# Kernel optimization log

Measured on AMD Instinct MI355X. Metric: run time of the kernel, lower is better.

The kernel has to match this reference:

```python
import jax, jax.numpy as jnp
import numpy as np

N = 100000   # nodes
C = 16       # num_classes
G = 2        # number of graphs (meta-paths)
L = 2        # PLP layers
E = 3200000  # edges per graph
F = 512      # feature dim
H = 64       # mlp hidden dim


def setup_inputs() -> dict:
    key = jax.random.key(0)
    ks = jax.random.split(key, 13)
    return {
        "features": jax.random.normal(ks[0], (N, F), jnp.float32),
        "label_init": jax.random.uniform(ks[1], (N, C), jnp.float32),
        "labels_one_hot": jax.random.uniform(ks[2], (N, C), jnp.float32),
        "alpha": jax.random.normal(ks[3], (N, 1), jnp.float32),
        "attention": jax.random.normal(ks[4], (N, G, 1), jnp.float32),
        "e_edge": jax.random.normal(ks[5], (L, G, E), jnp.float32),
        "w1": jax.random.normal(ks[6], (F, H), jnp.float32) * 0.05,
        "b1": jnp.zeros((H,), jnp.float32),
        "w2": jax.random.normal(ks[7], (H, C), jnp.float32) * 0.05,
        "b2": jnp.zeros((C,), jnp.float32),
        "src": jax.random.randint(ks[8], (G, E), 0, N, jnp.int32),
        "dst": jax.random.randint(ks[9], (G, E), 0, N, jnp.int32),
        "train_mask": jax.random.randint(ks[10], (N, 1), 0, 2, jnp.int32),
    }


def edge_softmax(e, dst, n):
    # softmax of per-edge logits over edges sharing the same destination node
    m = jax.ops.segment_max(e, dst, num_segments=n)          # [N]
    ex = jnp.exp(e - m[dst])                                  # [E]
    s = jax.ops.segment_sum(ex, dst, num_segments=n)          # [N]
    return ex / s[dst]


def reference(features, label_init, labels_one_hot, alpha, attention,
              e_edge, w1, b1, w2, b2, src, dst, train_mask):
    mask = train_mask.astype(jnp.float32)            # [N,1] 1 = train node
    masked_label = 1.0 - mask                         # (~masked).float()
    masked_one_hot = labels_one_hot * mask            # clamp train labels

    h_list = []
    for i in range(G):
        h = label_init
        for l in range(L):
            a = edge_softmax(e_edge[l, i], dst[i], N)         # [E]
            msg = h[src[i]] * a[:, None]                       # u_mul_e: [E,C]
            h = jax.ops.segment_sum(msg, dst[i], num_segments=N)  # fn.sum
            h = h * masked_label + masked_one_hot
        h_list.append(h)

    x = jnp.stack(h_list, axis=-1)                    # [N,C,G]
    att = jax.nn.softmax(attention, axis=1)[..., 0]   # [N,G]
    logits = jnp.einsum('ncg,ng->nc', x, att)         # [N,C]

    mlp_out = jax.nn.relu(features @ w1 + b1) @ w2 + b2   # MLP2, 2 layers
    return jax.nn.sigmoid(alpha) * logits + jax.nn.sigmoid(-alpha) * mlp_out
```

## Files before the change

### kernel.cpp

```cpp
#include <hip/hip_runtime.h>

#define NN 100000
#define CC 16
#define GG 2
#define LL 2
#define EE 3200000
#define FF 512
#define HH 64
#define GN (GG * NN)
#define GE (GG * EE)
#define CAPE (GE / 5 * 3)

#define SCAN_TILE 1024
#define SCAN_NB ((GN + SCAN_TILE - 1) / SCAN_TILE)

struct Pay { int src; float ex0; float ex1; };


__global__ __launch_bounds__(256) void count_kernel(
    const int* __restrict__ dst, const int* __restrict__ mask,
    int* __restrict__ deg)
{
    int t = blockIdx.x * 256 + threadIdx.x;
    int d = dst[t];
    if (mask[d] == 0) {
        int m = (t < EE ? 0 : NN) + d;
        atomicAdd(&deg[m], 1);
    }
}

__global__ __launch_bounds__(256) void scan_partial_kernel(
    const int* __restrict__ deg, int* __restrict__ bsum)
{
    __shared__ int lds[256];
    int t = threadIdx.x;
    int base = blockIdx.x * SCAN_TILE + t * 4;
    int s = 0;
    if (base + 3 < GN) {
        int4 v = *(const int4*)(deg + base);
        s = v.x + v.y + v.z + v.w;
    } else {
        for (int i = 0; i < 4; i++) if (base + i < GN) s += deg[base + i];
    }
    lds[t] = s;
    __syncthreads();
    for (int off = 128; off > 0; off >>= 1) {
        if (t < off) lds[t] += lds[t + off];
        __syncthreads();
    }
    if (t == 0) bsum[blockIdx.x] = lds[0];
}

__global__ __launch_bounds__(256) void scan_bsum_kernel(
    int* __restrict__ bsum, int* __restrict__ ptr)
{
    __shared__ int lds[256];
    int t = threadIdx.x;
    int v = (t < SCAN_NB) ? bsum[t] : 0;
    lds[t] = v;
    __syncthreads();
    for (int off = 1; off < 256; off <<= 1) {
        int y = (t >= off) ? lds[t - off] : 0;
        __syncthreads();
        lds[t] += y;
        __syncthreads();
    }
    if (t == 255) ptr[GN] = lds[255];
    bsum[t] = lds[t] - v;
}

__global__ __launch_bounds__(256) void scan_final_kernel(
    int* __restrict__ deg, const int* __restrict__ bsum, int* __restrict__ ptr)
{
    __shared__ int lds[256];
    int t = threadIdx.x;
    int base = blockIdx.x * SCAN_TILE + t * 4;
    int d0 = 0, d1 = 0, d2 = 0, d3 = 0;
    if (base + 3 < GN) {
        int4 v = *(const int4*)(deg + base);
        d0 = v.x; d1 = v.y; d2 = v.z; d3 = v.w;
    } else {
        if (base + 0 < GN) d0 = deg[base + 0];
        if (base + 1 < GN) d1 = deg[base + 1];
        if (base + 2 < GN) d2 = deg[base + 2];
        if (base + 3 < GN) d3 = deg[base + 3];
    }
    int s = d0 + d1 + d2 + d3;
    lds[t] = s;
    __syncthreads();
    for (int off = 1; off < 256; off <<= 1) {
        int y = (t >= off) ? lds[t - off] : 0;
        __syncthreads();
        lds[t] += y;
        __syncthreads();
    }
    int run = bsum[blockIdx.x] + lds[t] - s;
    if (base + 0 < GN) { ptr[base + 0] = run; deg[base + 0] = run; } run += d0;
    if (base + 1 < GN) { ptr[base + 1] = run; deg[base + 1] = run; } run += d1;
    if (base + 2 < GN) { ptr[base + 2] = run; deg[base + 2] = run; } run += d2;
    if (base + 3 < GN) { ptr[base + 3] = run; deg[base + 3] = run; }
}

__global__ __launch_bounds__(256) void scatter_kernel(
    const int* __restrict__ dst, const int* __restrict__ src,
    const float* __restrict__ e0, const float* __restrict__ e1,
    const int* __restrict__ mask, int* __restrict__ cursor,
    Pay* __restrict__ pay)
{
    int t = blockIdx.x * 256 + threadIdx.x;
    int d = dst[t];
    if (mask[d] != 0) return;
    int m = (t < EE ? 0 : NN) + d;
    int p = atomicAdd(&cursor[m], 1);
    if (p < CAPE) {
        Pay pv;
        pv.src = src[t];
        pv.ex0 = __expf(e0[t]);
        pv.ex1 = __expf(e1[t]);
        pay[p] = pv;
    }
}

__global__ __launch_bounds__(256) void gather_kernel(
    const Pay* __restrict__ pay, const int* __restrict__ ptr,
    const float* __restrict__ hs0, const float* __restrict__ hs1,
    const int* __restrict__ mask, const float* __restrict__ one_hot,
    float* __restrict__ hout, int layer)
{
    int m    = (blockIdx.x * 256 + threadIdx.x) >> 6;
    int lane = threadIdx.x & 63;
    int c    = lane & 15;
    int sub  = lane >> 4;
    int g    = (m < NN) ? 0 : 1;
    int n    = m - g * NN;

    if (mask[n]) {
        if (sub == 0) hout[m * CC + c] = one_hot[n * CC + c];
        return;
    }

    const float* hs = g ? hs1 : hs0;
    int beg = ptr[m], end = ptr[m + 1];
    float acc = 0.f, s = 0.f;
    for (int j = beg + sub; j < end; j += 4) {
        Pay pv = pay[j];
        float ex = layer ? pv.ex1 : pv.ex0;
        s   += ex;
        acc += ex * hs[pv.src * CC + c];
    }
    acc += __shfl_xor(acc, 16);
    acc += __shfl_xor(acc, 32);
    s   += __shfl_xor(s, 16);
    s   += __shfl_xor(s, 32);
    if (sub == 0)
        hout[m * CC + c] = (s > 0.f) ? acc / s : 0.f;
}

__global__ __launch_bounds__(256) void edge_kernel(
    const float* __restrict__ e, const int* __restrict__ src,
    const int* __restrict__ dst, const float* __restrict__ hs0,
    const float* __restrict__ hs1, float* __restrict__ hn,
    float* __restrict__ s)
{
    int t = blockIdx.x * 256 + threadIdx.x;
    int edge = t >> 4;
    int c = t & 15;
    float ev = e[edge];
    int sv = src[edge];
    int dv = dst[edge];
    float ex = __expf(ev);
    const float* hs;
    int hbase, sbase;
    if (edge < EE) { hs = hs0; hbase = 0;       sbase = 0;  }
    else           { hs = hs1; hbase = NN * CC; sbase = NN; }
    float val = hs[sv * CC + c] * ex;
    atomicAdd(&hn[hbase + dv * CC + c], val);
    if (c == 0) atomicAdd(&s[sbase + dv], ex);
}

__global__ __launch_bounds__(256) void update_kernel(
    const float* __restrict__ hn, const float* __restrict__ s,
    const int* __restrict__ train_mask, const float* __restrict__ labels_one_hot,
    float* __restrict__ hc)
{
    int idx = blockIdx.x * 256 + threadIdx.x;
    int n = idx >> 4;
    float mask = (float)train_mask[n];
    float ml = 1.0f - mask;
    float lab = labels_one_hot[idx] * mask;
#pragma unroll
    for (int g = 0; g < GG; g++) {
        float sv = s[g * NN + n];
        float x = (sv > 0.0f) ? hn[g * NN * CC + idx] / sv : 0.0f;
        hc[g * NN * CC + idx] = x * ml + lab;
    }
}

#define MLP_ROWS 128
__global__ __launch_bounds__(256) void mlp_combine_kernel(
    const float* __restrict__ feat, const float* __restrict__ w1,
    const float* __restrict__ b1, const float* __restrict__ w2,
    const float* __restrict__ b2, const float* __restrict__ hc,
    const float* __restrict__ attention, const float* __restrict__ alpha,
    float* __restrict__ out)
{
    __shared__ float smem[9792];
    float* sA  = smem;
    float* sB  = smem + 4224;
    float* sh1 = smem;
    float* sw2 = smem + 8704;

    int t = threadIdx.x;
    int row0 = blockIdx.x * MLP_ROWS;
    int rg = t >> 4;
    int cg = t & 15;

    for (int i = t; i < HH * CC; i += 256)
        sw2[(i >> 4) * 17 + (i & 15)] = w2[i];

    float acc[8][4];
#pragma unroll
    for (int r = 0; r < 8; r++)
#pragma unroll
        for (int c = 0; c < 4; c++) acc[r][c] = 0.0f;

    for (int kt = 0; kt < FF; kt += 32) {
#pragma unroll
        for (int i = 0; i < 4; i++) {
            int s4 = t + i * 256;
            int r  = s4 >> 3;
            int k4 = (s4 & 7) << 2;
            int grow = row0 + r;
            float4 v = make_float4(0.f, 0.f, 0.f, 0.f);
            if (grow < NN)
                v = *(const float4*)(feat + (size_t)grow * FF + kt + k4);
            sA[(k4 + 0) * 132 + r] = v.x;
            sA[(k4 + 1) * 132 + r] = v.y;
            sA[(k4 + 2) * 132 + r] = v.z;
            sA[(k4 + 3) * 132 + r] = v.w;
        }
#pragma unroll
        for (int i = 0; i < 2; i++) {
            int s4 = t + i * 256;
            int k  = s4 >> 4;
            int c4 = (s4 & 15) << 2;
            float4 wv = *(const float4*)(w1 + (size_t)(kt + k) * HH + c4);
            *(float4*)&sB[k * 68 + c4] = wv;
        }
        __syncthreads();
#pragma unroll 8
        for (int k = 0; k < 32; k++) {
            float4 a0 = *(const float4*)&sA[k * 132 + rg * 8];
            float4 a1 = *(const float4*)&sA[k * 132 + rg * 8 + 4];
            float4 b  = *(const float4*)&sB[k * 68 + cg * 4];
            float ar[8] = {a0.x, a0.y, a0.z, a0.w, a1.x, a1.y, a1.z, a1.w};
            float bc[4] = {b.x, b.y, b.z, b.w};
#pragma unroll
            for (int r = 0; r < 8; r++)
#pragma unroll
                for (int c = 0; c < 4; c++) acc[r][c] += ar[r] * bc[c];
        }
        __syncthreads();
    }

    float4 bb = *(const float4*)(b1 + cg * 4);
#pragma unroll
    for (int r = 0; r < 8; r++) {
        float4 hv;
        hv.x = fmaxf(acc[r][0] + bb.x, 0.f);
        hv.y = fmaxf(acc[r][1] + bb.y, 0.f);
        hv.z = fmaxf(acc[r][2] + bb.z, 0.f);
        hv.w = fmaxf(acc[r][3] + bb.w, 0.f);
        *(float4*)&sh1[(rg * 8 + r) * 68 + cg * 4] = hv;
    }
    __syncthreads();

    float acc2[8] = {0.f, 0.f, 0.f, 0.f, 0.f, 0.f, 0.f, 0.f};
    for (int k = 0; k < HH; k++) {
        float wv = sw2[k * 17 + cg];
#pragma unroll
        for (int r = 0; r < 8; r++)
            acc2[r] += sh1[(rg * 8 + r) * 68 + k] * wv;
    }

#pragma unroll
    for (int r = 0; r < 8; r++) {
        int row = row0 + rg * 8 + r;
        if (row < NN) {
            float mlp = acc2[r] + b2[cg];
            float a0 = attention[row * 2 + 0];
            float a1 = attention[row * 2 + 1];
            float t0 = 1.0f / (1.0f + __expf(a1 - a0));
            float h0 = hc[row * CC + cg];
            float h1 = hc[NN * CC + row * CC + cg];
            float logit = h0 * t0 + h1 * (1.0f - t0);
            float sa = 1.0f / (1.0f + __expf(-alpha[row]));
            out[row * CC + cg] = sa * logit + (1.0f - sa) * mlp;
        }
    }
}

extern "C" void kernel_launch(void* const* d_in, const int* in_sizes, int n_in,
                              void* d_out, int out_size, void* d_ws, size_t ws_size,
                              hipStream_t stream)
{
    const float* features       = (const float*)d_in[0];
    const float* label_init     = (const float*)d_in[1];
    const float* labels_one_hot = (const float*)d_in[2];
    const float* alpha          = (const float*)d_in[3];
    const float* attention      = (const float*)d_in[4];
    const float* e_edge         = (const float*)d_in[5];
    const float* w1             = (const float*)d_in[6];
    const float* b1             = (const float*)d_in[7];
    const float* w2             = (const float*)d_in[8];
    const float* b2             = (const float*)d_in[9];
    const int*   src            = (const int*)d_in[10];
    const int*   dst            = (const int*)d_in[11];
    const int*   train_mask     = (const int*)d_in[12];
    float* out = (float*)d_out;

    float* ws   = (float*)d_ws;
    float* h_a  = ws;
    float* h_b  = h_a + (size_t)GN * CC;
    Pay*   pay  = (Pay*)(h_b + (size_t)GN * CC);
    int*   ptr  = (int*)((char*)pay + (size_t)CAPE * sizeof(Pay));
    int*   deg  = ptr + GN + 4;
    int*   bsum = deg + GN;
    size_t need = (size_t)((char*)(bsum + 256) - (char*)d_ws);

    if (ws_size >= need) {
        hipMemsetAsync(deg, 0, (size_t)GN * sizeof(int), stream);
        count_kernel<<<GE / 256, 256, 0, stream>>>(dst, train_mask, deg);
        scan_partial_kernel<<<SCAN_NB, 256, 0, stream>>>(deg, bsum);
        scan_bsum_kernel<<<1, 256, 0, stream>>>(bsum, ptr);
        scan_final_kernel<<<SCAN_NB, 256, 0, stream>>>(deg, bsum, ptr);
        scatter_kernel<<<GE / 256, 256, 0, stream>>>(
            dst, src, e_edge, e_edge + (size_t)GE, train_mask, deg, pay);

        gather_kernel<<<(GN * 64) / 256, 256, 0, stream>>>(
            pay, ptr, label_init, label_init,
            train_mask, labels_one_hot, h_a, 0);
        gather_kernel<<<(GN * 64) / 256, 256, 0, stream>>>(
            pay, ptr, h_a, h_a + (size_t)NN * CC,
            train_mask, labels_one_hot, h_b, 1);

        mlp_combine_kernel<<<(NN + MLP_ROWS - 1) / MLP_ROWS, 256, 0, stream>>>(
            features, w1, b1, w2, b2, h_b, attention, alpha, out);
    } else {
        float* h_next = ws;
        float* s      = ws + (size_t)GG * NN * CC;
        float* h_cur  = s + (size_t)GG * NN;
        for (int l = 0; l < LL; l++) {
            hipMemsetAsync(h_next, 0,
                           ((size_t)GG * NN * CC + (size_t)GG * NN) * sizeof(float),
                           stream);
            const float* hs0 = (l == 0) ? label_init : h_cur;
            const float* hs1 = (l == 0) ? label_init : h_cur + (size_t)NN * CC;
            const float* ebase = e_edge + (size_t)l * GG * EE;
            edge_kernel<<<(2 * EE * 16) / 256, 256, 0, stream>>>(
                ebase, src, dst, hs0, hs1, h_next, s);
            update_kernel<<<(NN * CC) / 256, 256, 0, stream>>>(
                h_next, s, train_mask, labels_one_hot, h_cur);
        }
        mlp_combine_kernel<<<(NN + MLP_ROWS - 1) / MLP_ROWS, 256, 0, stream>>>(
            features, w1, b1, w2, b2, h_cur, attention, alpha, out);
    }
}
```

Baseline: 945.0 us.

## Replace per-node atomic scatter with two-pass bucketed CSR build

Edges are first scattered into 256-node buckets using one atomic cursor per bucket, with the local destination packed into the upper bits of src. A second kernel then reorders each bucket into exact per-node CSR positions using LDS atomics. The aim is to cut global atomic contention and make the scattered writes more local. The cost is an extra staging pass over roughly 3.4M payloads, with the staging buffer aliased onto the h buffers. The workspace layout changes, and the old atomic edge path is replaced by the previous CSR path as the fallback.

```diff
diff --git a/kernel.cpp b/kernel.cpp
--- a/kernel.cpp
+++ b/kernel.cpp
@@ -9,7 +9,10 @@
 #define HH 64
 #define GN (GG * NN)
 #define GE (GG * EE)
-#define CAPE (GE / 5 * 3)
+#define CAPE_FB (GE / 5 * 3)
+#define CAPE2 3400000
+#define BW 256
+#define NBUCK ((GN + BW - 1) / BW)
 
 #define SCAN_TILE 1024
 #define SCAN_NB ((GN + SCAN_TILE - 1) / SCAN_TILE)
@@ -101,6 +104,54 @@
     if (base + 3 < GN) { ptr[base + 3] = run; deg[base + 3] = run; }
 }
 
+__global__ __launch_bounds__(1024) void bcur_init_kernel(
+    const int* __restrict__ ptr, int* __restrict__ bcur)
+{
+    int b = threadIdx.x;
+    if (b < NBUCK) bcur[b] = ptr[b * BW];
+}
+
+__global__ __launch_bounds__(256) void bucket_scatter_kernel(
+    const int* __restrict__ dst, const int* __restrict__ src,
+    const float* __restrict__ e0, const float* __restrict__ e1,
+    const int* __restrict__ mask, int* __restrict__ bcur,
+    Pay* __restrict__ stag)
+{
+    int t = blockIdx.x * 256 + threadIdx.x;
+    int d = dst[t];
+    if (mask[d] != 0) return;
+    int m = (t < EE ? 0 : NN) + d;
+    int p = atomicAdd(&bcur[m >> 8], 1);
+    if (p < CAPE2) {
+        Pay pv;
+        pv.src = src[t] | ((m & 255) << 17);
+        pv.ex0 = __expf(e0[t]);
+        pv.ex1 = __expf(e1[t]);
+        stag[p] = pv;
+    }
+}
+
+__global__ __launch_bounds__(256) void bucket_order_kernel(
+    const Pay* __restrict__ stag, const int* __restrict__ ptr,
+    Pay* __restrict__ pay)
+{
+    __shared__ int cur[BW];
+    int b = blockIdx.x;
+    int t = threadIdx.x;
+    int nbase = b * BW;
+    cur[t] = (nbase + t < GN) ? ptr[nbase + t] : 0;
+    __syncthreads();
+    int beg = ptr[nbase];
+    int endIdx = nbase + BW; if (endIdx > GN) endIdx = GN;
+    int end = ptr[endIdx];
+    for (int i = beg + t; i < end; i += 256) {
+        Pay pv = stag[i];
+        int dl = (pv.src >> 17) & 255;
+        int slot = atomicAdd(&cur[dl], 1);
+        pay[slot] = pv;
+    }
+}
+
 __global__ __launch_bounds__(256) void scatter_kernel(
     const int* __restrict__ dst, const int* __restrict__ src,
     const float* __restrict__ e0, const float* __restrict__ e1,
@@ -112,7 +163,7 @@
     if (mask[d] != 0) return;
     int m = (t < EE ? 0 : NN) + d;
     int p = atomicAdd(&cursor[m], 1);
-    if (p < CAPE) {
+    if (p < CAPE_FB) {
         Pay pv;
         pv.src = src[t];
         pv.ex0 = __expf(e0[t]);
@@ -144,9 +195,10 @@
     float acc = 0.f, s = 0.f;
     for (int j = beg + sub; j < end; j += 4) {
         Pay pv = pay[j];
+        int sv = pv.src & 0x1FFFF;
         float ex = layer ? pv.ex1 : pv.ex0;
         s   += ex;
-        acc += ex * hs[pv.src * CC + c];
+        acc += ex * hs[sv * CC + c];
     }
     acc += __shfl_xor(acc, 16);
     acc += __shfl_xor(acc, 32);
@@ -154,46 +206,6 @@
     s   += __shfl_xor(s, 32);
     if (sub == 0)
         hout[m * CC + c] = (s > 0.f) ? acc / s : 0.f;
-}
-
-__global__ __launch_bounds__(256) void edge_kernel(
-    const float* __restrict__ e, const int* __restrict__ src,
-    const int* __restrict__ dst, const float* __restrict__ hs0,
-    const float* __restrict__ hs1, float* __restrict__ hn,
-    float* __restrict__ s)
-{
-    int t = blockIdx.x * 256 + threadIdx.x;
-    int edge = t >> 4;
-    int c = t & 15;
-    float ev = e[edge];
-    int sv = src[edge];
-    int dv = dst[edge];
-    float ex = __expf(ev);
-    const float* hs;
-    int hbase, sbase;
-    if (edge < EE) { hs = hs0; hbase = 0;       sbase = 0;  }
-    else           { hs = hs1; hbase = NN * CC; sbase = NN; }
-    float val = hs[sv * CC + c] * ex;
-    atomicAdd(&hn[hbase + dv * CC + c], val);
-    if (c == 0) atomicAdd(&s[sbase + dv], ex);
-}
-
-__global__ __launch_bounds__(256) void update_kernel(
-    const float* __restrict__ hn, const float* __restrict__ s,
-    const int* __restrict__ train_mask, const float* __restrict__ labels_one_hot,
-    float* __restrict__ hc)
-{
-    int idx = blockIdx.x * 256 + threadIdx.x;
-    int n = idx >> 4;
-    float mask = (float)train_mask[n];
-    float ml = 1.0f - mask;
-    float lab = labels_one_hot[idx] * mask;
-#pragma unroll
-    for (int g = 0; g < GG; g++) {
-        float sv = s[g * NN + n];
-        float x = (sv > 0.0f) ? hn[g * NN * CC + idx] / sv : 0.0f;
-        hc[g * NN * CC + idx] = x * ml + lab;
-    }
 }
 
 #define MLP_ROWS 128
@@ -318,15 +330,27 @@
     const int*   dst            = (const int*)d_in[11];
     const int*   train_mask     = (const int*)d_in[12];
     float* out = (float*)d_out;
-
-    float* ws   = (float*)d_ws;
-    float* h_a  = ws;
-    float* h_b  = h_a + (size_t)GN * CC;
-    Pay*   pay  = (Pay*)(h_b + (size_t)GN * CC);
-    int*   ptr  = (int*)((char*)pay + (size_t)CAPE * sizeof(Pay));
-    int*   deg  = ptr + GN + 4;
-    int*   bsum = deg + GN;
-    size_t need = (size_t)((char*)(bsum + 256) - (char*)d_ws);
+    const float* e0 = e_edge;
+    const float* e1 = e_edge + (size_t)GE;
+
+    char*  base  = (char*)d_ws;
+    Pay*   pay   = (Pay*)base;
+    int*   ptr   = (int*)(base + (size_t)CAPE2 * sizeof(Pay));
+    int*   deg   = ptr + GN + 4;
+    int*   bsum  = deg + GN;
+    int*   bcur  = bsum + 256;
+    Pay*   stag  = (Pay*)(bcur + 1024);
+    float* h_a   = (float*)stag;
+    float* h_b   = h_a + (size_t)GN * CC;
+    size_t need  = (size_t)((char*)(stag + (size_t)CAPE2) - base);
+
+    float* f_h_a  = (float*)base;
+    float* f_h_b  = f_h_a + (size_t)GN * CC;
+    Pay*   f_pay  = (Pay*)(f_h_b + (size_t)GN * CC);
+    int*   f_ptr  = (int*)((char*)f_pay + (size_t)CAPE_FB * sizeof(Pay));
+    int*   f_deg  = f_ptr + GN + 4;
+    int*   f_bsum = f_deg + GN;
+    size_t need_fb = (size_t)((char*)(f_bsum + 256) - base);
 
     if (ws_size >= need) {
         hipMemsetAsync(deg, 0, (size_t)GN * sizeof(int), stream);
@@ -334,8 +358,10 @@
         scan_partial_kernel<<<SCAN_NB, 256, 0, stream>>>(deg, bsum);
         scan_bsum_kernel<<<1, 256, 0, stream>>>(bsum, ptr);
         scan_final_kernel<<<SCAN_NB, 256, 0, stream>>>(deg, bsum, ptr);
-        scatter_kernel<<<GE / 256, 256, 0, stream>>>(
-            dst, src, e_edge, e_edge + (size_t)GE, train_mask, deg, pay);
+        bcur_init_kernel<<<1, 1024, 0, stream>>>(ptr, bcur);
+        bucket_scatter_kernel<<<GE / 256, 256, 0, stream>>>(
+            dst, src, e0, e1, train_mask, bcur, stag);
+        bucket_order_kernel<<<NBUCK, 256, 0, stream>>>(stag, ptr, pay);
 
         gather_kernel<<<(GN * 64) / 256, 256, 0, stream>>>(
             pay, ptr, label_init, label_init,
@@ -346,23 +372,23 @@
 
         mlp_combine_kernel<<<(NN + MLP_ROWS - 1) / MLP_ROWS, 256, 0, stream>>>(
             features, w1, b1, w2, b2, h_b, attention, alpha, out);
-    } else {
-        float* h_next = ws;
-        float* s      = ws + (size_t)GG * NN * CC;
-        float* h_cur  = s + (size_t)GG * NN;
-        for (int l = 0; l < LL; l++) {
-            hipMemsetAsync(h_next, 0,
-                           ((size_t)GG * NN * CC + (size_t)GG * NN) * sizeof(float),
-                           stream);
-            const float* hs0 = (l == 0) ? label_init : h_cur;
-            const float* hs1 = (l == 0) ? label_init : h_cur + (size_t)NN * CC;
-            const float* ebase = e_edge + (size_t)l * GG * EE;
-            edge_kernel<<<(2 * EE * 16) / 256, 256, 0, stream>>>(
-                ebase, src, dst, hs0, hs1, h_next, s);
-            update_kernel<<<(NN * CC) / 256, 256, 0, stream>>>(
-                h_next, s, train_mask, labels_one_hot, h_cur);
-        }
+    } else if (ws_size >= need_fb) {
+        hipMemsetAsync(f_deg, 0, (size_t)GN * sizeof(int), stream);
+        count_kernel<<<GE / 256, 256, 0, stream>>>(dst, train_mask, f_deg);
+        scan_partial_kernel<<<SCAN_NB, 256, 0, stream>>>(f_deg, f_bsum);
+        scan_bsum_kernel<<<1, 256, 0, stream>>>(f_bsum, f_ptr);
+        scan_final_kernel<<<SCAN_NB, 256, 0, stream>>>(f_deg, f_bsum, f_ptr);
+        scatter_kernel<<<GE / 256, 256, 0, stream>>>(
+            dst, src, e0, e1, train_mask, f_deg, f_pay);
+
+        gather_kernel<<<(GN * 64) / 256, 256, 0, stream>>>(
+            f_pay, f_ptr, label_init, label_init,
+            train_mask, labels_one_hot, f_h_a, 0);
+        gather_kernel<<<(GN * 64) / 256, 256, 0, stream>>>(
+            f_pay, f_ptr, f_h_a, f_h_a + (size_t)NN * CC,
+            train_mask, labels_one_hot, f_h_b, 1);
+
         mlp_combine_kernel<<<(NN + MLP_ROWS - 1) / MLP_ROWS, 256, 0, stream>>>(
-            features, w1, b1, w2, b2, h_cur, attention, alpha, out);
-    }
-}
+            features, w1, b1, w2, b2, f_h_b, attention, alpha, out);
+    }
+}
```

After: 2.180 ms. +130.7%, slower.
